# Kernel optimization log

Measured on AMD Instinct MI355X. Metric: run time of the kernel, lower is better.

Reference implementation:

```python
import jax, jax.numpy as jnp
import numpy as np

NOISE_DB = 40.0  # layer's `noise` ctor arg (SNR in dB)


def setup_inputs() -> dict:
    key = jax.random.key(0)
    k1, k2, k3 = jax.random.split(key, 3)
    B, M, L, S = 4, 256, 24, 22  # S = shots = round(M*L/(M+L-1))
    x = jax.random.normal(k1, (B, M, M, L), dtype=jnp.float32)
    # coded aperture weights, init N(0,1)/sqrt(kern*kern) as in build()
    H = jax.random.normal(k2, (1, M, M, 1, S), dtype=jnp.float32) / np.float32(M)
    # standard-normal noise sample (the layer draws this internally)
    noise_eps = jax.random.normal(k3, (B, M, M + L - 1, 1), dtype=jnp.float32)
    return {"x": x, "H": H, "noise_eps": noise_eps}


def reference(x, H, noise_eps):
    B, M, _, L = x.shape
    S = H.shape[-1]
    W = M + L - 1  # dispersed detector width
    H2 = H[0, :, :, 0, :]  # (M, M, S)

    # Aux1 = H * x : (B, M, M, L, S)
    HX = H2[None, :, :, None, :] * x[..., None]

    # Forward shear-sum: Y[b,m,n,s] = sum_i HX[b,m,n-i,i,s]
    # (equivalent to the pad + L rolls + extract-band-i + reduce_sum)
    Y = jnp.zeros((B, M, W, S), dtype=x.dtype)
    for i in range(L):  # fixed small spectral loop; indexed accumulation, no padded rolls
        Y = Y.at[:, :, i:i + M, :].add(HX[:, :, :, i, :])

    # Noise: sigma^2 = ||Y||^2 / (M * W * B * 10^(noise/10)); broadcast over shots
    sigm = jnp.sum(Y * Y) / (M * W * B * (10.0 ** (NOISE_DB / 10.0)))
    Y = Y + jnp.sqrt(sigm) * noise_eps  # noise_eps: (B, M, W, 1)

    # Reverse shift-extract: X[b,m,n,i] = sum_s H2[m,n,s] * Y[b,m,n+i,s]
    Ys = jnp.stack([Y[:, :, i:i + M, :] for i in range(L)], axis=3)  # (B,M,M,L,S)
    X = jnp.einsum('bmnls,mns->bmnl', Ys, H2)

    return X / jnp.max(X)
```

## Files before the change

kernel.cpp:

```cpp
#include <hip/hip_runtime.h>
#include <math.h>

namespace {
constexpr int Mz = 256, Lz = 24, Sz = 22, Bz = 4;
constexpr int Wz = Mz + Lz - 1;
constexpr int ST = 23;
constexpr int TOT = Bz * Mz * Mz * Lz;
constexpr double SIGM_DEN = (double)Mz * (double)Wz * (double)Bz * 1e4;
}

__device__ __forceinline__ unsigned int enc_f32(float f) {
  unsigned int u = __float_as_uint(f);
  return (u & 0x80000000u) ? ~u : (u | 0x80000000u);
}
__device__ __forceinline__ float dec_f32(unsigned int e) {
  unsigned int u = (e & 0x80000000u) ? (e ^ 0x80000000u) : ~e;
  return __uint_as_float(u);
}

__global__ __launch_bounds__(256) void k_init(const float* __restrict__ H,
                                              float* __restrict__ hsum,
                                              double* __restrict__ sumsq,
                                              unsigned int* __restrict__ maxenc)
{
  int idx = blockIdx.x * 256 + threadIdx.x;
  if (idx == 0) { *sumsq = 0.0; *maxenc = 0u; }
  if (idx < Mz * Mz) {
    const float* __restrict__ hp = H + (size_t)idx * Sz;
    float a = 0.f;
    #pragma unroll
    for (int s = 0; s < Sz; ++s) a += hp[s];
    hsum[idx] = a;
  }
}

__global__ __launch_bounds__(256) void k_fwd(const float* __restrict__ x,
                                             const float* __restrict__ H,
                                             float* __restrict__ X0,
                                             double* __restrict__ sumsq)
{
  __shared__ float Hs[Mz * ST];
  __shared__ float Ys[Wz * ST];
  __shared__ float xs[Mz * Lz];
  __shared__ double wred[4];

  const int b = blockIdx.x >> 8;
  const int m = blockIdx.x & 255;
  const float* __restrict__ xp = x + (size_t)(b * Mz + m) * (Mz * Lz);
  const float* __restrict__ Hp = H + (size_t)m * (Mz * Sz);

  for (int e = threadIdx.x; e < Mz * Sz; e += 256) {
    int n = e / Sz, s = e - n * Sz;
    Hs[n * ST + s] = Hp[e];
  }
  for (int e = threadIdx.x; e < Mz * Lz; e += 256) xs[e] = xp[e];
  __syncthreads();

  double local = 0.0;
  for (int w = threadIdx.x; w < Wz; w += 256) {
    int i0 = w - (Mz - 1); if (i0 < 0) i0 = 0;
    int i1 = w;            if (i1 > Lz - 1) i1 = Lz - 1;
    float acc[Sz];
    #pragma unroll
    for (int s = 0; s < Sz; ++s) acc[s] = 0.f;
    for (int i = i0; i <= i1; ++i) {
      const int n = w - i;
      const float xv = xs[n * Lz + i];
      const float* __restrict__ hrow = &Hs[n * ST];
      #pragma unroll
      for (int s = 0; s < Sz; ++s) acc[s] = fmaf(hrow[s], xv, acc[s]);
    }
    float* __restrict__ yrow = &Ys[w * ST];
    #pragma unroll
    for (int s = 0; s < Sz; ++s) {
      yrow[s] = acc[s];
      local += (double)acc[s] * (double)acc[s];
    }
  }
  __syncthreads();

  for (int off = 32; off > 0; off >>= 1) local += __shfl_down(local, off, 64);
  const int lane = threadIdx.x & 63, wid = threadIdx.x >> 6;
  if (lane == 0) wred[wid] = local;
  __syncthreads();
  if (threadIdx.x == 0) atomicAdd(sumsq, wred[0] + wred[1] + wred[2] + wred[3]);

  float* __restrict__ Xp = X0 + (size_t)(b * Mz + m) * (Mz * Lz);
  for (int e = threadIdx.x; e < Mz * Lz; e += 256) {
    const int n = e / Lz, l = e - n * Lz;
    const float* __restrict__ yrow = &Ys[(n + l) * ST];
    const float* __restrict__ hrow = &Hs[n * ST];
    float acc = 0.f;
    #pragma unroll
    for (int s = 0; s < Sz; ++s) acc = fmaf(yrow[s], hrow[s], acc);
    Xp[e] = acc;
  }
}

__global__ __launch_bounds__(256) void k_max(const float* __restrict__ X0,
                                             const float* __restrict__ eps,
                                             const float* __restrict__ hsum,
                                             const double* __restrict__ sumsq,
                                             unsigned int* __restrict__ maxenc)
{
  const float c = sqrtf((float)(*sumsq / SIGM_DEN));
  float mx = -3.4e38f;
  const int stride = gridDim.x * 256;
  for (int e = blockIdx.x * 256 + threadIdx.x; e < TOT; e += stride) {
    const int l = e % Lz;
    const int t = e / Lz;
    const int n = t & 255;
    const int bm = t >> 8;
    const int m = bm & 255;
    const float v = X0[e] + c * eps[bm * Wz + n + l] * hsum[(m << 8) + n];
    mx = fmaxf(mx, v);
  }
  for (int off = 32; off > 0; off >>= 1) mx = fmaxf(mx, __shfl_down(mx, off, 64));
  __shared__ float wred[4];
  const int lane = threadIdx.x & 63, wid = threadIdx.x >> 6;
  if (lane == 0) wred[wid] = mx;
  __syncthreads();
  if (threadIdx.x == 0) {
    float bmx = fmaxf(fmaxf(wred[0], wred[1]), fmaxf(wred[2], wred[3]));
    atomicMax(maxenc, enc_f32(bmx));
  }
}

__global__ __launch_bounds__(256) void k_final(float* __restrict__ Xio,
                                               const float* __restrict__ eps,
                                               const float* __restrict__ hsum,
                                               const double* __restrict__ sumsq,
                                               const unsigned int* __restrict__ maxenc)
{
  const float c = sqrtf((float)(*sumsq / SIGM_DEN));
  const float mx = dec_f32(*maxenc);
  const int stride = gridDim.x * 256;
  for (int e = blockIdx.x * 256 + threadIdx.x; e < TOT; e += stride) {
    const int l = e % Lz;
    const int t = e / Lz;
    const int n = t & 255;
    const int bm = t >> 8;
    const int m = bm & 255;
    const float v = Xio[e] + c * eps[bm * Wz + n + l] * hsum[(m << 8) + n];
    Xio[e] = v / mx;
  }
}

extern "C" void kernel_launch(void* const* d_in, const int* in_sizes, int n_in,
                              void* d_out, int out_size, void* d_ws, size_t ws_size,
                              hipStream_t stream) {
  const float* x   = (const float*)d_in[0];
  const float* H   = (const float*)d_in[1];
  const float* eps = (const float*)d_in[2];
  float* out = (float*)d_out;

  double*       sumsq  = (double*)d_ws;
  unsigned int* maxenc = (unsigned int*)((char*)d_ws + 8);
  float*        hsum   = (float*)((char*)d_ws + 16);

  k_init <<<(Mz * Mz + 255) / 256, 256, 0, stream>>>(H, hsum, sumsq, maxenc);
  k_fwd  <<<Bz * Mz,              256, 0, stream>>>(x, H, out, sumsq);
  k_max  <<<1024,                 256, 0, stream>>>(out, eps, hsum, sumsq, maxenc);
  k_final<<<1024,                 256, 0, stream>>>(out, eps, hsum, sumsq, maxenc);
}
```

Before: 152.2 us.

## Fuse max and normalize via grid barrier, vectorize and widen forward kernel

```diff
diff --git a/kernel.cpp b/kernel.cpp
--- a/kernel.cpp
+++ b/kernel.cpp
@@ -4,8 +4,9 @@
 namespace {
 constexpr int Mz = 256, Lz = 24, Sz = 22, Bz = 4;
 constexpr int Wz = Mz + Lz - 1;
-constexpr int ST = 23;
-constexpr int TOT = Bz * Mz * Mz * Lz;
+constexpr int HST = 22;
+constexpr int XST = 25;
+constexpr int NBLK = Bz * Mz;
 constexpr double SIGM_DEN = (double)Mz * (double)Wz * (double)Bz * 1e4;
 }
 
@@ -21,129 +22,168 @@
 __global__ __launch_bounds__(256) void k_init(const float* __restrict__ H,
                                               float* __restrict__ hsum,
                                               double* __restrict__ sumsq,
-                                              unsigned int* __restrict__ maxenc)
+                                              unsigned int* __restrict__ maxenc,
+                                              unsigned int* __restrict__ bar)
 {
   int idx = blockIdx.x * 256 + threadIdx.x;
-  if (idx == 0) { *sumsq = 0.0; *maxenc = 0u; }
+  if (idx == 0) { *sumsq = 0.0; *maxenc = 0u; *bar = 0u; }
   if (idx < Mz * Mz) {
-    const float* __restrict__ hp = H + (size_t)idx * Sz;
+    const float2* __restrict__ hp = (const float2*)(H + (size_t)idx * Sz);
     float a = 0.f;
     #pragma unroll
-    for (int s = 0; s < Sz; ++s) a += hp[s];
+    for (int k = 0; k < 11; ++k) { float2 h = hp[k]; a += h.x + h.y; }
     hsum[idx] = a;
   }
 }
 
-__global__ __launch_bounds__(256) void k_fwd(const float* __restrict__ x,
-                                             const float* __restrict__ H,
-                                             float* __restrict__ X0,
-                                             double* __restrict__ sumsq)
+__global__ __launch_bounds__(512, 4) void k_fwd(const float* __restrict__ x,
+                                                const float* __restrict__ H,
+                                                float* __restrict__ X0,
+                                                double* __restrict__ sumsq)
 {
-  __shared__ float Hs[Mz * ST];
-  __shared__ float Ys[Wz * ST];
-  __shared__ float xs[Mz * Lz];
-  __shared__ double wred[4];
-
+  __shared__ __align__(16) float Hs[Mz * HST];
+  __shared__ __align__(16) float Ys[Wz * HST];
+  __shared__ __align__(16) float xs[Mz * XST];
+  __shared__ double wred[8];
+
+  const int tid = threadIdx.x;
   const int b = blockIdx.x >> 8;
   const int m = blockIdx.x & 255;
   const float* __restrict__ xp = x + (size_t)(b * Mz + m) * (Mz * Lz);
   const float* __restrict__ Hp = H + (size_t)m * (Mz * Sz);
 
-  for (int e = threadIdx.x; e < Mz * Sz; e += 256) {
-    int n = e / Sz, s = e - n * Sz;
-    Hs[n * ST + s] = Hp[e];
-  }
-  for (int e = threadIdx.x; e < Mz * Lz; e += 256) xs[e] = xp[e];
+  {
+    const float4* __restrict__ src = (const float4*)Hp;
+    float4* dst = (float4*)Hs;
+    #pragma unroll 3
+    for (int e = tid; e < Mz * HST / 4; e += 512) dst[e] = src[e];
+  }
+  #pragma unroll 3
+  for (int e = tid; e < Mz * Lz / 4; e += 512) {
+    float4 v = ((const float4*)xp)[e];
+    int j = 4 * e, r = j / 24, c = j - r * 24;
+    float* d = &xs[r * XST + c];
+    d[0] = v.x; d[1] = v.y; d[2] = v.z; d[3] = v.w;
+  }
   __syncthreads();
 
   double local = 0.0;
-  for (int w = threadIdx.x; w < Wz; w += 256) {
-    int i0 = w - (Mz - 1); if (i0 < 0) i0 = 0;
-    int i1 = w;            if (i1 > Lz - 1) i1 = Lz - 1;
-    float acc[Sz];
-    #pragma unroll
-    for (int s = 0; s < Sz; ++s) acc[s] = 0.f;
+  for (int w = tid; w < Wz; w += 512) {
+    const int i0 = (w > Mz - 1) ? (w - (Mz - 1)) : 0;
+    const int i1 = (w < Lz - 1) ? w : (Lz - 1);
+    float2 acc[11];
+    #pragma unroll
+    for (int k = 0; k < 11; ++k) acc[k] = make_float2(0.f, 0.f);
     for (int i = i0; i <= i1; ++i) {
       const int n = w - i;
-      const float xv = xs[n * Lz + i];
-      const float* __restrict__ hrow = &Hs[n * ST];
+      const float xv = xs[n * XST + i];
+      const float2* __restrict__ hrow = (const float2*)&Hs[n * HST];
       #pragma unroll
-      for (int s = 0; s < Sz; ++s) acc[s] = fmaf(hrow[s], xv, acc[s]);
-    }
-    float* __restrict__ yrow = &Ys[w * ST];
-    #pragma unroll
-    for (int s = 0; s < Sz; ++s) {
-      yrow[s] = acc[s];
-      local += (double)acc[s] * (double)acc[s];
-    }
-  }
-  __syncthreads();
+      for (int k = 0; k < 11; ++k) {
+        float2 h = hrow[k];
+        acc[k].x = fmaf(h.x, xv, acc[k].x);
+        acc[k].y = fmaf(h.y, xv, acc[k].y);
+      }
+    }
+    float2* yrow = (float2*)&Ys[w * HST];
+    #pragma unroll
+    for (int k = 0; k < 11; ++k) {
+      yrow[k] = acc[k];
+      local += (double)acc[k].x * acc[k].x + (double)acc[k].y * acc[k].y;
+    }
+  }
 
   for (int off = 32; off > 0; off >>= 1) local += __shfl_down(local, off, 64);
-  const int lane = threadIdx.x & 63, wid = threadIdx.x >> 6;
+  const int lane = tid & 63, wid = tid >> 6;
   if (lane == 0) wred[wid] = local;
   __syncthreads();
-  if (threadIdx.x == 0) atomicAdd(sumsq, wred[0] + wred[1] + wred[2] + wred[3]);
-
-  float* __restrict__ Xp = X0 + (size_t)(b * Mz + m) * (Mz * Lz);
-  for (int e = threadIdx.x; e < Mz * Lz; e += 256) {
-    const int n = e / Lz, l = e - n * Lz;
-    const float* __restrict__ yrow = &Ys[(n + l) * ST];
-    const float* __restrict__ hrow = &Hs[n * ST];
-    float acc = 0.f;
-    #pragma unroll
-    for (int s = 0; s < Sz; ++s) acc = fmaf(yrow[s], hrow[s], acc);
-    Xp[e] = acc;
-  }
-}
-
-__global__ __launch_bounds__(256) void k_max(const float* __restrict__ X0,
-                                             const float* __restrict__ eps,
-                                             const float* __restrict__ hsum,
-                                             const double* __restrict__ sumsq,
-                                             unsigned int* __restrict__ maxenc)
+  if (tid == 0) {
+    double s = 0.0;
+    #pragma unroll
+    for (int k = 0; k < 8; ++k) s += wred[k];
+    atomicAdd(sumsq, s);
+  }
+
+  {
+    const int n = tid >> 1;
+    const int l0 = (tid & 1) * 12;
+    const float2* __restrict__ hr2 = (const float2*)&Hs[n * HST];
+    float hr[22];
+    #pragma unroll
+    for (int k = 0; k < 11; ++k) { float2 h = hr2[k]; hr[2*k] = h.x; hr[2*k+1] = h.y; }
+    float outv[12];
+    #pragma unroll
+    for (int j = 0; j < 12; ++j) {
+      const float2* __restrict__ yr = (const float2*)&Ys[(n + l0 + j) * HST];
+      float a0 = 0.f, a1 = 0.f;
+      #pragma unroll
+      for (int k = 0; k < 11; ++k) {
+        float2 y = yr[k];
+        a0 = fmaf(y.x, hr[2*k],   a0);
+        a1 = fmaf(y.y, hr[2*k+1], a1);
+      }
+      outv[j] = a0 + a1;
+    }
+    float4* __restrict__ Xp4 =
+        (float4*)(X0 + (size_t)(b * Mz + m) * (Mz * Lz) + tid * 12);
+    Xp4[0] = make_float4(outv[0], outv[1], outv[2],  outv[3]);
+    Xp4[1] = make_float4(outv[4], outv[5], outv[6],  outv[7]);
+    Xp4[2] = make_float4(outv[8], outv[9], outv[10], outv[11]);
+  }
+}
+
+__global__ __launch_bounds__(256, 4) void k_maxfinal(float* __restrict__ Xio,
+                                                     const float* __restrict__ eps,
+                                                     const float* __restrict__ hsum,
+                                                     const double* __restrict__ sumsq,
+                                                     unsigned int* __restrict__ maxenc,
+                                                     unsigned int* __restrict__ bar)
 {
   const float c = sqrtf((float)(*sumsq / SIGM_DEN));
+  const int n = threadIdx.x;
+  const int bm = blockIdx.x;
+  const int m = bm & 255;
+  float* __restrict__ row = Xio + (size_t)bm * (Mz * Lz) + n * Lz;
+  const float* __restrict__ ep = eps + bm * Wz + n;
+  const float hv = c * hsum[(m << 8) + n];
+
+  float v[24];
+  {
+    const float4* __restrict__ r4 = (const float4*)row;
+    #pragma unroll
+    for (int q = 0; q < 6; ++q) {
+      float4 t = r4[q];
+      v[4*q+0] = t.x; v[4*q+1] = t.y; v[4*q+2] = t.z; v[4*q+3] = t.w;
+    }
+  }
   float mx = -3.4e38f;
-  const int stride = gridDim.x * 256;
-  for (int e = blockIdx.x * 256 + threadIdx.x; e < TOT; e += stride) {
-    const int l = e % Lz;
-    const int t = e / Lz;
-    const int n = t & 255;
-    const int bm = t >> 8;
-    const int m = bm & 255;
-    const float v = X0[e] + c * eps[bm * Wz + n + l] * hsum[(m << 8) + n];
-    mx = fmaxf(mx, v);
-  }
+  #pragma unroll
+  for (int l = 0; l < 24; ++l) {
+    v[l] = fmaf(hv, ep[l], v[l]);
+    mx = fmaxf(mx, v[l]);
+  }
+
   for (int off = 32; off > 0; off >>= 1) mx = fmaxf(mx, __shfl_down(mx, off, 64));
-  __shared__ float wred[4];
-  const int lane = threadIdx.x & 63, wid = threadIdx.x >> 6;
-  if (lane == 0) wred[wid] = mx;
-  __syncthreads();
-  if (threadIdx.x == 0) {
-    float bmx = fmaxf(fmaxf(wred[0], wred[1]), fmaxf(wred[2], wred[3]));
+  __shared__ float wredf[4];
+  __shared__ unsigned int smax;
+  const int lane = n & 63, wid = n >> 6;
+  if (lane == 0) wredf[wid] = mx;
+  __syncthreads();
+  if (n == 0) {
+    float bmx = fmaxf(fmaxf(wredf[0], wredf[1]), fmaxf(wredf[2], wredf[3]));
     atomicMax(maxenc, enc_f32(bmx));
-  }
-}
-
-__global__ __launch_bounds__(256) void k_final(float* __restrict__ Xio,
-                                               const float* __restrict__ eps,
-                                               const float* __restrict__ hsum,
-                                               const double* __restrict__ sumsq,
-                                               const unsigned int* __restrict__ maxenc)
-{
-  const float c = sqrtf((float)(*sumsq / SIGM_DEN));
-  const float mx = dec_f32(*maxenc);
-  const int stride = gridDim.x * 256;
-  for (int e = blockIdx.x * 256 + threadIdx.x; e < TOT; e += stride) {
-    const int l = e % Lz;
-    const int t = e / Lz;
-    const int n = t & 255;
-    const int bm = t >> 8;
-    const int m = bm & 255;
-    const float v = Xio[e] + c * eps[bm * Wz + n + l] * hsum[(m << 8) + n];
-    Xio[e] = v / mx;
-  }
+    __threadfence();
+    __hip_atomic_fetch_add(bar, 1u, __ATOMIC_ACQ_REL, __HIP_MEMORY_SCOPE_AGENT);
+    while (__hip_atomic_load(bar, __ATOMIC_ACQUIRE, __HIP_MEMORY_SCOPE_AGENT) < (unsigned)NBLK) {}
+    smax = __hip_atomic_load(maxenc, __ATOMIC_ACQUIRE, __HIP_MEMORY_SCOPE_AGENT);
+  }
+  __syncthreads();
+
+  const float inv = 1.0f / dec_f32(smax);
+  float4* __restrict__ w4 = (float4*)row;
+  #pragma unroll
+  for (int q = 0; q < 6; ++q)
+    w4[q] = make_float4(v[4*q+0]*inv, v[4*q+1]*inv, v[4*q+2]*inv, v[4*q+3]*inv);
 }
 
 extern "C" void kernel_launch(void* const* d_in, const int* in_sizes, int n_in,
@@ -156,10 +196,10 @@
 
   double*       sumsq  = (double*)d_ws;
   unsigned int* maxenc = (unsigned int*)((char*)d_ws + 8);
+  unsigned int* bar    = (unsigned int*)((char*)d_ws + 12);
   float*        hsum   = (float*)((char*)d_ws + 16);
 
-  k_init <<<(Mz * Mz + 255) / 256, 256, 0, stream>>>(H, hsum, sumsq, maxenc);
-  k_fwd  <<<Bz * Mz,              256, 0, stream>>>(x, H, out, sumsq);
-  k_max  <<<1024,                 256, 0, stream>>>(out, eps, hsum, sumsq, maxenc);
-  k_final<<<1024,                 256, 0, stream>>>(out, eps, hsum, sumsq, maxenc);
-}
+  k_init     <<<(Mz * Mz + 255) / 256, 256, 0, stream>>>(H, hsum, sumsq, maxenc, bar);
+  k_fwd      <<<NBLK, 512, 0, stream>>>(x, H, out, sumsq);
+  k_maxfinal <<<NBLK, 256, 0, stream>>>(out, eps, hsum, sumsq, maxenc, bar);
+}
```

Result: slower. 225.3 us (+48.0%).
